# Kernel optimization log

Measured on AMD Instinct MI355X. Metric: run time of the kernel, lower is better.

Reference implementation:

```python
import jax, jax.numpy as jnp
import numpy as np

D_MODEL = 2048
N_HEADS = 8
N_KV = 4
HEAD_DIM = 256
WINDOW = 1024
EPS = 1e-6
ROPE_BASE = 10000.0


def _rms_norm(x, w):
    # x: [..., D]; matches torch: x * rsqrt(mean(x^2) + eps) * w
    return x * jax.lax.rsqrt(jnp.mean(x * x, axis=-1, keepdims=True) + EPS) * w


def _rope_cos_sin(pos):
    # pos: [T] ints -> cos/sin: [T, HEAD_DIM] (cat(freqs, freqs) as in source)
    inv_freq = 1.0 / (ROPE_BASE ** (jnp.arange(0, HEAD_DIM, 2, dtype=jnp.float32) / HEAD_DIM))
    freqs = pos.astype(jnp.float32)[:, None] * inv_freq[None, :]  # [T, D/2]
    emb = jnp.concatenate([freqs, freqs], axis=-1)                # [T, D]
    return jnp.cos(emb), jnp.sin(emb)


def _apply_rotary(x, cos, sin):
    # x: [B, H, T, D]; interleaved rotate-half exactly as the torch code
    x1 = x[..., 0::2]
    x2 = x[..., 1::2]
    x_rot = jnp.stack([-x2, x1], axis=-1).reshape(x.shape)
    return x * cos[None, None, :, :] + x_rot * sin[None, None, :, :]


def setup_inputs() -> dict:
    key = jax.random.key(0)
    ks = jax.random.split(key, 8)
    B, T = 1, 4096
    s = 0.02
    return {
        "x": jax.random.normal(ks[0], (B, T, D_MODEL), dtype=jnp.float32),
        "pos": jnp.arange(T, dtype=jnp.int32),
        "Wq": jax.random.normal(ks[1], (N_HEADS * HEAD_DIM, D_MODEL), dtype=jnp.float32) * s,
        "Wk": jax.random.normal(ks[2], (N_KV * HEAD_DIM, D_MODEL), dtype=jnp.float32) * s,
        "Wv": jax.random.normal(ks[3], (N_KV * HEAD_DIM, D_MODEL), dtype=jnp.float32) * s,
        "Wo": jax.random.normal(ks[4], (D_MODEL, N_HEADS * HEAD_DIM), dtype=jnp.float32) * s,
        "q_norm_w": jnp.ones((HEAD_DIM,), dtype=jnp.float32),
        "k_norm_w": jnp.ones((HEAD_DIM,), dtype=jnp.float32),
    }


def reference(x, pos, Wq, Wk, Wv, Wo, q_norm_w, k_norm_w):
    B, T, _ = x.shape
    # projections (torch Linear: y = x @ W.T)
    q = (x @ Wq.T).reshape(B, T, N_HEADS, HEAD_DIM).transpose(0, 2, 1, 3)  # [B,H,T,D]
    k = (x @ Wk.T).reshape(B, T, N_KV, HEAD_DIM).transpose(0, 2, 1, 3)    # [B,Hkv,T,D]
    v = (x @ Wv.T).reshape(B, T, N_KV, HEAD_DIM).transpose(0, 2, 1, 3)
    # per-head RMSNorm
    q = _rms_norm(q, q_norm_w)
    k = _rms_norm(k, k_norm_w)
    # RoPE
    cos, sin = _rope_cos_sin(pos)
    q = _apply_rotary(q, cos, sin)
    k = _apply_rotary(k, cos, sin)
    # GQA repeat: [B,Hkv,T,D] -> [B,H,T,D]
    rep = N_HEADS // N_KV
    k = jnp.repeat(k, rep, axis=1)
    v = jnp.repeat(v, rep, axis=1)
    # full scores + sliding-window causal mask (faithful to source)
    scores = jnp.einsum("bhqd,bhkd->bhqk", q, k) / jnp.sqrt(jnp.float32(HEAD_DIM))
    i = jnp.arange(T)[:, None]
    j = jnp.arange(T)[None, :]
    allowed = (j <= i) & (j >= i - WINDOW + 1)  # [T,T]
    scores = jnp.where(allowed[None, None, :, :], scores, -jnp.inf)
    attn = jax.nn.softmax(scores, axis=-1)
    y = jnp.einsum("bhqk,bhkd->bhqd", attn, v)
    y = y.transpose(0, 2, 1, 3).reshape(B, T, N_HEADS * HEAD_DIM)
    return y @ Wo.T
```

## Files before the change

### kernel.cpp

```cpp
#include <hip/hip_runtime.h>
#include <cstdint>
#include <cmath>

typedef __bf16 bf16x8 __attribute__((ext_vector_type(8)));
typedef float  f32x4  __attribute__((ext_vector_type(4)));

#define DEVI __device__ __forceinline__

#define SEQ 4096
#define NH 8
#define NKV 4
#define HD 256
#define WIN 1024

DEVI void gload16(const void* g, void* l) {
  __builtin_amdgcn_global_load_lds((const __attribute__((address_space(1))) void*)g,
                                   (__attribute__((address_space(3))) void*)l,
                                   16, 0, 0);
}

DEVI bf16x8 ld8f(const float* p) {
  const f32x4 a = *(const f32x4*)p;
  const f32x4 b = *(const f32x4*)(p + 4);
  bf16x8 r;
#pragma unroll
  for (int j = 0; j < 4; ++j) { r[j] = (__bf16)a[j]; r[4 + j] = (__bf16)b[j]; }
  return r;
}

DEVI void st1(float* p, float v)  { *p = v; }
DEVI void st1(__bf16* p, float v) { *p = (__bf16)v; }

__global__ __launch_bounds__(256)
void cvt_all(const float* __restrict__ x,  const float* __restrict__ wq,
             const float* __restrict__ wk, const float* __restrict__ wv,
             const float* __restrict__ wo,
             __bf16* __restrict__ xb, __bf16* __restrict__ wqkvb,
             __bf16* __restrict__ wob) {
  const size_t g = (size_t)blockIdx.x * 256 + threadIdx.x;
  const float* src; __bf16* dst; size_t off;
  if      (g < 1048576) { src = x;  dst = xb;               off = g; }
  else if (g < 1572864) { src = wq; dst = wqkvb;            off = g - 1048576; }
  else if (g < 1835008) { src = wk; dst = wqkvb + 4194304;  off = g - 1572864; }
  else if (g < 2097152) { src = wv; dst = wqkvb + 6291456;  off = g - 1835008; }
  else                  { src = wo; dst = wob;              off = g - 2097152; }
  *(bf16x8*)(dst + off * 8) = ld8f(src + off * 8);
}

template <typename TC>
__global__ __launch_bounds__(256, 2)
void gemm_bt(const __bf16* __restrict__ A, const __bf16* __restrict__ B,
             TC* __restrict__ C, int N, int K) {
  __shared__ __bf16 As2[2][128][32];
  __shared__ __bf16 Bs2[2][128][32];
  const int tid  = threadIdx.x;
  const int lane = tid & 63;
  const int wave = tid >> 6;
  const int l15  = lane & 15;
  const int l4   = lane >> 4;

  const int lin  = blockIdx.x + gridDim.x * blockIdx.y;
  const int xcd  = lin & 7;
  const int kk   = lin >> 3;
  const int row0 = (xcd * 4 + (kk & 3)) * 128;
  const int col0 = (kk >> 2) * 128;

  const int wm   = (wave >> 1) * 64;
  const int wn   = (wave & 1) * 64;

  f32x4 acc[4][4] = {};

  for (int k0 = 0; k0 < K; k0 += 64) {
    __syncthreads();
#pragma unroll
    for (int i = 0; i < 4; ++i) {
      const int s  = i * 256 + tid;
      const int ch = s >> 9, r = (s >> 2) & 127, c4 = s & 3;
      gload16(A + (size_t)(row0 + r) * K + k0 + ch * 32 + c4 * 8,
              (char*)As2 + (i * 256 + wave * 64) * 16);
    }
#pragma unroll
    for (int i = 0; i < 4; ++i) {
      const int s  = i * 256 + tid;
      const int ch = s >> 9, r = (s >> 2) & 127, c4 = s & 3;
      gload16(B + (size_t)(col0 + r) * K + k0 + ch * 32 + c4 * 8,
              (char*)Bs2 + (i * 256 + wave * 64) * 16);
    }
    __syncthreads();
#pragma unroll
    for (int ch = 0; ch < 2; ++ch) {
      bf16x8 af[4], bfr[4];
#pragma unroll
      for (int i = 0; i < 4; ++i)
        af[i] = *(const bf16x8*)&As2[ch][wm + i * 16 + l15][l4 * 8];
#pragma unroll
      for (int i = 0; i < 4; ++i)
        bfr[i] = *(const bf16x8*)&Bs2[ch][wn + i * 16 + l15][l4 * 8];
#pragma unroll
      for (int i = 0; i < 4; ++i)
#pragma unroll
        for (int j = 0; j < 4; ++j)
          acc[i][j] = __builtin_amdgcn_mfma_f32_16x16x32_bf16(af[i], bfr[j], acc[i][j], 0, 0, 0);
    }
  }

#pragma unroll
  for (int i = 0; i < 4; ++i) {
#pragma unroll
    for (int reg = 0; reg < 4; ++reg) {
      const int row = row0 + wm + i * 16 + l4 * 4 + reg;
      TC* crow = C + (size_t)row * N + col0 + wn + l15;
#pragma unroll
      for (int j = 0; j < 4; ++j)
        st1(crow + j * 16, acc[i][j][reg]);
    }
  }
}

__global__ __launch_bounds__(256)
void norm_rope_tv(__bf16* __restrict__ qkv, __bf16* __restrict__ Vt,
                  const float* __restrict__ qw, const float* __restrict__ kw,
                  const int* __restrict__ pos) {
  if (blockIdx.x < 12288) {
    const int gw   = blockIdx.x * 4 + (threadIdx.x >> 6);
    const int lane = threadIdx.x & 63;
    __bf16* base; const float* w; int t;
    if (gw < SEQ * NH) {
      t = gw >> 3;
      base = qkv + (size_t)t * 4096 + (gw & 7) * HD;
      w = qw;
    } else {
      const int g = gw - SEQ * NH;
      t = g >> 2;
      base = qkv + (size_t)t * 4096 + 2048 + (g & 3) * HD;
      w = kw;
    }

    const int d0 = lane * 4;
    float v[4]; float ss = 0.f;
#pragma unroll
    for (int j = 0; j < 4; ++j) { v[j] = (float)base[d0 + j]; ss += v[j] * v[j]; }
#pragma unroll
    for (int off = 1; off < 64; off <<= 1) ss += __shfl_xor(ss, off);
    const float rms = rsqrtf(ss * (1.0f / 256.0f) + 1e-6f);
    const float p = (float)pos[t];

    float n[4];
#pragma unroll
    for (int j = 0; j < 4; ++j) n[j] = v[j] * rms * w[d0 + j];

    float outv[4];
#pragma unroll
    for (int e = 0; e < 4; e += 2) {
      const int i0 = d0 + e, i1 = i0 + 1;
      const float f0 = exp2f(-(float)(i0 & 127) * 0.103810253f);
      const float f1 = exp2f(-(float)(i1 & 127) * 0.103810253f);
      float s0, cc0, s1, cc1;
      sincosf(p * f0, &s0, &cc0);
      sincosf(p * f1, &s1, &cc1);
      outv[e]     = n[e] * cc0 - n[e + 1] * s0;
      outv[e + 1] = n[e + 1] * cc1 + n[e] * s1;
    }
#pragma unroll
    for (int j = 0; j < 4; ++j) base[d0 + j] = (__bf16)outv[j];
  } else {
    __shared__ __bf16 tile[64][72];
    const int b   = blockIdx.x - 12288;
    const int tid = threadIdx.x;
    const int tb  = (b & 63) * 64;
    const int yy  = b >> 6;
    const int kvh = yy >> 2;
    const int db  = (yy & 3) * 64;
#pragma unroll
    for (int i = 0; i < 2; ++i) {
      const int s = i * 256 + tid;
      const int r = s >> 3, c = (s & 7) * 8;
      bf16x8 val = *(const bf16x8*)(qkv + (size_t)(tb + r) * 4096 + 3072 + kvh * HD + db + c);
#pragma unroll
      for (int j = 0; j < 8; ++j) tile[r][c + j] = val[j];
    }
    __syncthreads();
#pragma unroll
    for (int i = 0; i < 2; ++i) {
      const int s = i * 256 + tid;
      const int r = s >> 3, c = (s & 7) * 8;
      bf16x8 outv;
#pragma unroll
      for (int j = 0; j < 8; ++j) outv[j] = tile[c + j][r];
      *(bf16x8*)(Vt + (size_t)(kvh * HD + db + r) * SEQ + tb + c) = outv;
    }
  }
}

__global__ __launch_bounds__(256, 2)
void attn_fwd(const __bf16* __restrict__ qkv, const __bf16* __restrict__ Vt,
              __bf16* __restrict__ Y) {
  __shared__ __bf16 Ks2[8][64][32];
  __shared__ __bf16 Vts2[2][256][32];
  __shared__ __bf16 Ps[4][16][72];
  const int tid  = threadIdx.x;
  const int lane = tid & 63;
  const int wave = tid >> 6;
  const int l15  = lane & 15;
  const int l4   = lane >> 4;
  const int q0   = blockIdx.x * 64;
  const int head = blockIdx.y;
  const int kvh  = head >> 1;
  const int qw   = q0 + wave * 16;

  bf16x8 qf[8];
  const __bf16* qrow = qkv + (size_t)(qw + l15) * 4096 + head * HD;
#pragma unroll
  for (int ks = 0; ks < 8; ++ks) {
    bf16x8 t = *(const bf16x8*)(qrow + ks * 32 + l4 * 8);
#pragma unroll
    for (int j = 0; j < 8; ++j) t[j] = (__bf16)((float)t[j] * 0.0625f);
    qf[ks] = t;
  }

  f32x4 o[16] = {};
  float l_run[4] = {0.f, 0.f, 0.f, 0.f};

  int lo = q0 - (WIN - 1); if (lo < 0) lo = 0;
  const int kt0 = lo >> 6;
  const int kt1 = (q0 + 63) >> 6;

  for (int kt = kt0; kt <= kt1; ++kt) {
    const int kb = kt * 64;
    __syncthreads();
#pragma unroll
    for (int i = 0; i < 8; ++i) {
      const int s = i * 256 + tid;
      gload16(qkv + (size_t)(kb + ((s >> 2) & 63)) * 4096 + 2048 + kvh * HD
                  + (s >> 8) * 32 + (s & 3) * 8,
              (char*)Ks2 + (i * 256 + wave * 64) * 16);
    }
#pragma unroll
    for (int i = 0; i < 8; ++i) {
      const int s = i * 256 + tid;
      gload16(Vt + ((size_t)kvh * HD + ((s >> 2) & 255)) * SEQ + kb
                 + (s >> 10) * 32 + (s & 3) * 8,
              (char*)Vts2 + (i * 256 + wave * 64) * 16);
    }
    __syncthreads();

    f32x4 s_acc[4] = {};
#pragma unroll
    for (int kn = 0; kn < 4; ++kn) {
#pragma unroll
      for (int ks = 0; ks < 8; ++ks) {
        bf16x8 kf = *(const bf16x8*)&Ks2[ks][kn * 16 + l15][l4 * 8];
        s_acc[kn] = __builtin_amdgcn_mfma_f32_16x16x32_bf16(qf[ks], kf, s_acc[kn], 0, 0, 0);
      }
    }

#pragma unroll
    for (int reg = 0; reg < 4; ++reg) {
      const int r  = l4 * 4 + reg;
      const int qg = qw + r;
      float ps = 0.f;
#pragma unroll
      for (int kn = 0; kn < 4; ++kn) {
        const int kg = kb + kn * 16 + l15;
        const bool ok = (kg <= qg) && (kg > qg - WIN);
        const float p = ok ? __expf(fminf(s_acc[kn][reg], 34.f) - 34.f) : 0.f;
        ps += p;
        Ps[wave][r][kn * 16 + l15] = (__bf16)p;
      }
      l_run[reg] += ps;
    }

#pragma unroll
    for (int ks2 = 0; ks2 < 2; ++ks2) {
      bf16x8 pf = *(const bf16x8*)&Ps[wave][l15][ks2 * 32 + l4 * 8];
#pragma unroll
      for (int dn = 0; dn < 16; ++dn) {
        bf16x8 vf = *(const bf16x8*)&Vts2[ks2][dn * 16 + l15][l4 * 8];
        o[dn] = __builtin_amdgcn_mfma_f32_16x16x32_bf16(pf, vf, o[dn], 0, 0, 0);
      }
    }
  }

#pragma unroll
  for (int reg = 0; reg < 4; ++reg) {
#pragma unroll
    for (int off = 1; off < 16; off <<= 1)
      l_run[reg] += __shfl_xor(l_run[reg], off);
    const float inv = 1.0f / l_run[reg];
    const int q = qw + l4 * 4 + reg;
    __bf16* yrow = Y + ((size_t)q * NH + head) * HD + l15;
#pragma unroll
    for (int dn = 0; dn < 16; ++dn)
      yrow[dn * 16] = (__bf16)(o[dn][reg] * inv);
  }
}

extern "C" void kernel_launch(void* const* d_in, const int* in_sizes, int n_in,
                              void* d_out, int out_size, void* d_ws, size_t ws_size,
                              hipStream_t stream) {
  (void)in_sizes; (void)n_in; (void)out_size; (void)ws_size;
  const float* x   = (const float*)d_in[0];
  const int*   pos = (const int*)d_in[1];
  const float* Wq  = (const float*)d_in[2];
  const float* Wk  = (const float*)d_in[3];
  const float* Wv  = (const float*)d_in[4];
  const float* Wo  = (const float*)d_in[5];
  const float* qw  = (const float*)d_in[6];
  const float* kw  = (const float*)d_in[7];
  float* out = (float*)d_out;

  char* ws = (char*)d_ws;
  const size_t MB = 1024 * 1024;
  __bf16* qkv_ws = (__bf16*)(ws);
  __bf16* vt_ws  = (__bf16*)(ws + 32 * MB);
  __bf16* y_ws   = (__bf16*)(ws + 40 * MB);
  __bf16* xb     = (__bf16*)(ws + 56 * MB);
  __bf16* wqkvb  = (__bf16*)(ws + 72 * MB);
  __bf16* wob    = (__bf16*)(ws + 88 * MB);

  cvt_all<<<dim3(10240), dim3(256), 0, stream>>>(x, Wq, Wk, Wv, Wo, xb, wqkvb, wob);
  gemm_bt<__bf16><<<dim3(32, 32), dim3(256), 0, stream>>>(xb, wqkvb, qkv_ws, 4096, 2048);
  norm_rope_tv<<<dim3(13312), dim3(256), 0, stream>>>(qkv_ws, vt_ws, qw, kw, pos);
  attn_fwd<<<dim3(64, 8), dim3(256), 0, stream>>>(qkv_ws, vt_ws, y_ws);
  gemm_bt<float><<<dim3(32, 16), dim3(256), 0, stream>>>(y_ws, wob, out, 2048, 2048);
}
```

Before: 331.5 us.

## Replace GEMM with 256-wide tiles, swizzled LDS and multi-stage async prefetch

Replaces the 128x128 bf16 GEMM used for both the QKV and output projections with a 512-thread kernel using 256x256 (QKV) or 128x256 (output) tiles. It adds a double-buffered, half-K staged direct-to-LDS prefetch pipeline with explicit vmcnt waits and raw barriers, XOR-swizzled LDS addressing to avoid bank conflicts, and raised wave priority around the MFMA block. The goal is more reuse per loaded tile and hiding global-load latency behind matrix math. In exchange it uses far more LDS and registers per block, and the grid shrinks to 256 blocks, which can limit occupancy.

```diff
diff --git a/kernel.cpp b/kernel.cpp
--- a/kernel.cpp
+++ b/kernel.cpp
@@ -30,6 +30,12 @@
 
 DEVI void st1(float* p, float v)  { *p = v; }
 DEVI void st1(__bf16* p, float v) { *p = (__bf16)v; }
+
+DEVI void barx() {
+  asm volatile("" ::: "memory");
+  __builtin_amdgcn_s_barrier();
+  asm volatile("" ::: "memory");
+}
 
 __global__ __launch_bounds__(256)
 void cvt_all(const float* __restrict__ x,  const float* __restrict__ wq,
@@ -47,72 +53,112 @@
   *(bf16x8*)(dst + off * 8) = ld8f(src + off * 8);
 }
 
-template <typename TC>
-__global__ __launch_bounds__(256, 2)
-void gemm_bt(const __bf16* __restrict__ A, const __bf16* __restrict__ B,
+template <int BM, typename TC>
+__global__ __launch_bounds__(512, 2)
+void gemm256(const __bf16* __restrict__ A, const __bf16* __restrict__ B,
              TC* __restrict__ C, int N, int K) {
-  __shared__ __bf16 As2[2][128][32];
-  __shared__ __bf16 Bs2[2][128][32];
+  constexpr int AI    = BM / 128;
+  constexpr int MF    = BM / 32;
+  constexpr int AUNIT = BM * 64;
+  constexpr int ASZ   = 4 * AUNIT;
+  constexpr int VMC   = 2 * (AI + 2);
+  __shared__ char lds[ASZ + 65536];
+
   const int tid  = threadIdx.x;
   const int lane = tid & 63;
   const int wave = tid >> 6;
   const int l15  = lane & 15;
   const int l4   = lane >> 4;
-
-  const int lin  = blockIdx.x + gridDim.x * blockIdx.y;
+  const int wm   = wave >> 2;
+  const int wn   = wave & 3;
+
+  constexpr int nTm = 4096 / BM;
+  const int lin  = blockIdx.x;
   const int xcd  = lin & 7;
   const int kk   = lin >> 3;
-  const int row0 = (xcd * 4 + (kk & 3)) * 128;
-  const int col0 = (kk >> 2) * 128;
-
-  const int wm   = (wave >> 1) * 64;
-  const int wn   = (wave & 1) * 64;
-
-  f32x4 acc[4][4] = {};
-
-  for (int k0 = 0; k0 < K; k0 += 64) {
-    __syncthreads();
-#pragma unroll
-    for (int i = 0; i < 4; ++i) {
-      const int s  = i * 256 + tid;
-      const int ch = s >> 9, r = (s >> 2) & 127, c4 = s & 3;
-      gload16(A + (size_t)(row0 + r) * K + k0 + ch * 32 + c4 * 8,
-              (char*)As2 + (i * 256 + wave * 64) * 16);
-    }
-#pragma unroll
-    for (int i = 0; i < 4; ++i) {
-      const int s  = i * 256 + tid;
-      const int ch = s >> 9, r = (s >> 2) & 127, c4 = s & 3;
-      gload16(B + (size_t)(col0 + r) * K + k0 + ch * 32 + c4 * 8,
-              (char*)Bs2 + (i * 256 + wave * 64) * 16);
-    }
-    __syncthreads();
-#pragma unroll
-    for (int ch = 0; ch < 2; ++ch) {
-      bf16x8 af[4], bfr[4];
-#pragma unroll
-      for (int i = 0; i < 4; ++i)
-        af[i] = *(const bf16x8*)&As2[ch][wm + i * 16 + l15][l4 * 8];
-#pragma unroll
-      for (int i = 0; i < 4; ++i)
-        bfr[i] = *(const bf16x8*)&Bs2[ch][wn + i * 16 + l15][l4 * 8];
-#pragma unroll
-      for (int i = 0; i < 4; ++i)
-#pragma unroll
-        for (int j = 0; j < 4; ++j)
-          acc[i][j] = __builtin_amdgcn_mfma_f32_16x16x32_bf16(af[i], bfr[j], acc[i][j], 0, 0, 0);
-    }
-  }
-
-#pragma unroll
-  for (int i = 0; i < 4; ++i) {
+  const int nTn  = N >> 8;
+  const int rowT = kk % nTm;
+  const int colT = xcd * (nTn >> 3) + kk / nTm;
+  const int row0 = rowT * BM;
+  const int col0 = colT << 8;
+
+  const int srow = tid >> 2;
+  const int scol = ((tid & 3) ^ ((tid >> 3) & 3)) << 3;
+  const __bf16* Asrc = A + (size_t)(row0 + srow) * K + scol;
+  const __bf16* Bsrc = B + (size_t)(col0 + srow) * K + scol;
+
+  const int swz  = (l4 ^ ((l15 >> 1) & 3)) << 4;
+  const int aoff = (wm * (BM / 2) + l15) * 64 + swz;
+  const int boff = ((wn << 6) + l15) * 64 + swz;
+
+  auto stA = [&](int kx, int h, int b) {
+    int k0 = kx << 6; if (k0 >= K) k0 = 0;
+    const __bf16* s = Asrc + k0 + (h << 5);
+    char* d = lds + (b * 2 + h) * AUNIT + wave * 1024;
+#pragma unroll
+    for (int i = 0; i < AI; ++i)
+      gload16(s + (size_t)(i << 7) * K, d + i * 8192);
+  };
+  auto stB = [&](int kx, int h, int b) {
+    int k0 = kx << 6; if (k0 >= K) k0 = 0;
+    const __bf16* s = Bsrc + k0 + (h << 5);
+    char* d = lds + ASZ + (b * 2 + h) * 16384 + wave * 1024;
+#pragma unroll
+    for (int i = 0; i < 2; ++i)
+      gload16(s + (size_t)(i << 7) * K, d + i * 8192);
+  };
+
+  f32x4 acc[MF][4] = {};
+
+  stA(0, 0, 0); stB(0, 0, 0);
+  stA(0, 1, 0); stB(0, 1, 0);
+  stA(1, 0, 1); stB(1, 0, 1);
+
+  const int NT = K >> 6;
+  for (int kt = 0; kt < NT; ++kt) {
+    const int b = kt & 1, nb = b ^ 1;
+#pragma unroll
+    for (int half = 0; half < 2; ++half) {
+      asm volatile("s_waitcnt vmcnt(%0)" :: "i"(VMC) : "memory");
+      barx();
+      bf16x8 af[4], ag[4], bfr[4];
+      const char* pa = lds + (b * 2 + half) * AUNIT + aoff;
+      const char* pb = lds + ASZ + (b * 2 + half) * 16384 + boff;
+#pragma unroll
+      for (int m = 0; m < 4; ++m) af[m] = *(const bf16x8*)(pa + (m << 10));
+#pragma unroll
+      for (int n = 0; n < 4; ++n) bfr[n] = *(const bf16x8*)(pb + (n << 10));
+      if constexpr (BM == 256) {
+#pragma unroll
+        for (int m = 0; m < 4; ++m) ag[m] = *(const bf16x8*)(pa + 4096 + (m << 10));
+      }
+      if (half == 0) { stA(kt + 1, 1, nb); stB(kt + 1, 1, nb); }
+      else           { stA(kt + 2, 0, b);  stB(kt + 2, 0, b);  }
+      __builtin_amdgcn_s_setprio(1);
+#pragma unroll
+      for (int m = 0; m < 4; ++m)
+#pragma unroll
+        for (int n = 0; n < 4; ++n)
+          acc[m][n] = __builtin_amdgcn_mfma_f32_16x16x32_bf16(af[m], bfr[n], acc[m][n], 0, 0, 0);
+      if constexpr (BM == 256) {
+#pragma unroll
+        for (int m = 0; m < 4; ++m)
+#pragma unroll
+          for (int n = 0; n < 4; ++n)
+            acc[4 + m][n] = __builtin_amdgcn_mfma_f32_16x16x32_bf16(ag[m], bfr[n], acc[4 + m][n], 0, 0, 0);
+      }
+      __builtin_amdgcn_s_setprio(0);
+    }
+  }
+
+#pragma unroll
+  for (int mf = 0; mf < MF; ++mf) {
+    const int rb = row0 + wm * (BM / 2) + (mf >> 2) * 64 + (mf & 3) * 16 + (l4 << 2);
 #pragma unroll
     for (int reg = 0; reg < 4; ++reg) {
-      const int row = row0 + wm + i * 16 + l4 * 4 + reg;
-      TC* crow = C + (size_t)row * N + col0 + wn + l15;
-#pragma unroll
-      for (int j = 0; j < 4; ++j)
-        st1(crow + j * 16, acc[i][j][reg]);
+      TC* crow = C + (size_t)(rb + reg) * N + col0 + (wn << 6) + l15;
+#pragma unroll
+      for (int n = 0; n < 4; ++n) st1(crow + (n << 4), acc[mf][n][reg]);
     }
   }
 }
@@ -319,8 +365,8 @@
   __bf16* wob    = (__bf16*)(ws + 88 * MB);
 
   cvt_all<<<dim3(10240), dim3(256), 0, stream>>>(x, Wq, Wk, Wv, Wo, xb, wqkvb, wob);
-  gemm_bt<__bf16><<<dim3(32, 32), dim3(256), 0, stream>>>(xb, wqkvb, qkv_ws, 4096, 2048);
+  gemm256<256, __bf16><<<dim3(256), dim3(512), 0, stream>>>(xb, wqkvb, qkv_ws, 4096, 2048);
   norm_rope_tv<<<dim3(13312), dim3(256), 0, stream>>>(qkv_ws, vt_ws, qw, kw, pos);
   attn_fwd<<<dim3(64, 8), dim3(256), 0, stream>>>(qkv_ws, vt_ws, y_ws);
-  gemm_bt<float><<<dim3(32, 16), dim3(256), 0, stream>>>(y_ws, wob, out, 2048, 2048);
-}
+  gemm256<128, float><<<dim3(256), dim3(512), 0, stream>>>(y_ws, wob, out, 2048, 2048);
+}
```

Result: faster. 318.3 us (-4.0%).
